# Kernel tuning notes

Hardware: AMD Instinct MI355X
Metric: run time of the kernel (lower is better)

## Reference

```python
import jax, jax.numpy as jnp
import numpy as np

K = 3          # kernel_size
DEG_P = 6      # numerator coeffs (order 5)
DEG_Q = 4      # denominator coeffs (powers 1..4)


def setup_inputs() -> dict:
    key = jax.random.key(0)
    k1, k2, k3 = jax.random.split(key, 3)
    B, Cin, Cout, H, W = 4, 16, 16, 64, 64
    x = jax.random.normal(k1, (B, Cin, H, W), dtype=jnp.float32)
    # per (out_channel f, in_channel c, kernel position p) rational coefficients
    A = jax.random.normal(k2, (Cout, Cin, K * K, DEG_P), dtype=jnp.float32) * 0.1
    Bc = jax.random.normal(k3, (Cout, Cin, K * K, DEG_Q), dtype=jnp.float32) * 0.1
    return {"x": x, "A": A, "Bc": Bc}


def reference(x, A, Bc):
    # x: [B, C, H, W]; A: [F, C, K*K, 6]; Bc: [F, C, K*K, 4]
    B, C, H, W = x.shape
    pad = (K - 1) // 2
    xp = jnp.pad(x, ((0, 0), (0, 0), (pad, pad), (pad, pad)))
    # sliding windows, one slice per kernel offset -> [K*K, B, C, H, W]
    wins = jnp.stack([xp[:, :, i:i + H, j:j + W]
                      for i in range(K) for j in range(K)])
    # powers x^0..x^5 -> [K*K, B, C, H, W, 6]
    pw = wins[..., None] ** jnp.arange(DEG_P, dtype=x.dtype)
    P = jnp.einsum('pbchwi,fcpi->fpbchw', pw, A)
    Q = 1.0 + jnp.abs(jnp.einsum('pbchwi,fcpi->fpbchw', pw[..., 1:1 + DEG_Q], Bc))
    # sum over kernel positions (p) and input channels (c) -> [F, B, H, W]
    out = jnp.sum(P / Q, axis=(1, 3))
    return jnp.transpose(out, (1, 0, 2, 3))  # [B, F, H, W]
```

## Files before the change

### kernel.cpp

```cpp
#include <hip/hip_runtime.h>


#define BB   4
#define CIN  16
#define COUT 16
#define HH   64
#define WW   64

__global__ __launch_bounds__(1024, 8) void KAConv_kernel(
    const float* __restrict__ x,
    const float* __restrict__ A,
    const float* __restrict__ Bc,
    float* __restrict__ out)
{
    const int blk = blockIdx.x;
    const int f   = blk & 15;
    const int rp  = (blk >> 4) & 31;
    const int b   = blk >> 9;

    const int tid  = threadIdx.x;
    const int cw   = __builtin_amdgcn_readfirstlane(tid >> 6);
    const int lane = tid & 63;
    const int w    = lane;
    const int r0   = rp << 1;

    const float* __restrict__ Ac = A  + (f * CIN + cw) * 54;
    const float* __restrict__ Bq = Bc + (f * CIN + cw) * 36;
    const float* __restrict__ xc = x  + (b * CIN + cw) * (HH * WW);

    float vv[4][3];
    #pragma unroll
    for (int ri = 0; ri < 4; ++ri) {
        const int hh   = r0 - 1 + ri;
        const bool okh = (hh >= 0) & (hh < HH);
        #pragma unroll
        for (int j = 0; j < 3; ++j) {
            const int wj  = w + j - 1;
            const bool ok = okh & (wj >= 0) & (wj < WW);
            vv[ri][j] = ok ? xc[hh * WW + wj] : 0.0f;
        }
    }

    float acc0 = 0.0f, acc1 = 0.0f;

    #pragma unroll
    for (int p = 0; p < 9; ++p) {
        const int i = p / 3;
        const int j = p % 3;
        const float va = vv[i][j];
        const float vb = vv[i + 1][j];
        const float a0 = Ac[p * 6 + 0], a1 = Ac[p * 6 + 1], a2 = Ac[p * 6 + 2];
        const float a3 = Ac[p * 6 + 3], a4 = Ac[p * 6 + 4], a5 = Ac[p * 6 + 5];
        const float b1 = Bq[p * 4 + 0], b2 = Bq[p * 4 + 1];
        const float b3 = Bq[p * 4 + 2], b4 = Bq[p * 4 + 3];

        float P0 = a5, P1 = a5;
        P0 = fmaf(P0, va, a4);  P1 = fmaf(P1, vb, a4);
        P0 = fmaf(P0, va, a3);  P1 = fmaf(P1, vb, a3);
        P0 = fmaf(P0, va, a2);  P1 = fmaf(P1, vb, a2);
        P0 = fmaf(P0, va, a1);  P1 = fmaf(P1, vb, a1);
        P0 = fmaf(P0, va, a0);  P1 = fmaf(P1, vb, a0);

        float q0 = b4, q1 = b4;
        q0 = fmaf(q0, va, b3);  q1 = fmaf(q1, vb, b3);
        q0 = fmaf(q0, va, b2);  q1 = fmaf(q1, vb, b2);
        q0 = fmaf(q0, va, b1);  q1 = fmaf(q1, vb, b1);
        q0 *= va;               q1 *= vb;

        const float d0 = 1.0f + fabsf(q0);
        const float d1 = 1.0f + fabsf(q1);
        acc0 = fmaf(P0, __builtin_amdgcn_rcpf(d0), acc0);
        acc1 = fmaf(P1, __builtin_amdgcn_rcpf(d1), acc1);
    }

    __shared__ float sRed[CIN][128];
    sRed[cw][lane]      = acc0;
    sRed[cw][64 + lane] = acc1;
    __syncthreads();

    if (tid < 128) {
        float s = 0.0f;
        #pragma unroll
        for (int k = 0; k < CIN; ++k) s += sRed[k][tid];
        const int row = r0 + (tid >> 6);
        const int col = tid & 63;
        out[((b * COUT + f) * HH + row) * WW + col] = s;
    }
}

extern "C" void kernel_launch(void* const* d_in, const int* in_sizes, int n_in,
                              void* d_out, int out_size, void* d_ws, size_t ws_size,
                              hipStream_t stream) {
    const float* x  = (const float*)d_in[0];
    const float* A  = (const float*)d_in[1];
    const float* Bc = (const float*)d_in[2];
    float* out = (float*)d_out;

    const int grid = BB * (HH / 2) * COUT;
    KAConv_kernel<<<grid, 1024, 0, stream>>>(x, A, Bc, out);
}
```

Measured before the change: 19.97 us.

## Pair rational terms over common denominator and widen per-block row tiling

Each block now computes 8 output rows with 512 threads, and each wave processes two input channels over a 10-row register window, so loaded input rows are reused across rows. Pairs of kernel-position terms are combined as (PA*dB+PB*dA)/(dA*dB), which roughly halves the reciprocal instructions. This adds a few multiplies and may raise register pressure. It also risks precision loss or overflow in the product of denominators for large inputs.

Measured after the change: 23.38 us. +17.1%, slower.

```diff
diff --git a/kernel.cpp b/kernel.cpp
--- a/kernel.cpp
+++ b/kernel.cpp
@@ -7,7 +7,24 @@
 #define HH   64
 #define WW   64
 
-__global__ __launch_bounds__(1024, 8) void KAConv_kernel(
+static __device__ __forceinline__ void rat(const float* __restrict__ Ac,
+                                           const float* __restrict__ Bq,
+                                           int p, float v, float& P, float& d)
+{
+    const float a0 = Ac[p*6+0], a1 = Ac[p*6+1], a2 = Ac[p*6+2];
+    const float a3 = Ac[p*6+3], a4 = Ac[p*6+4], a5 = Ac[p*6+5];
+    const float b1 = Bq[p*4+0], b2 = Bq[p*4+1], b3 = Bq[p*4+2], b4 = Bq[p*4+3];
+    float Pp = a5;
+    Pp = fmaf(Pp, v, a4); Pp = fmaf(Pp, v, a3); Pp = fmaf(Pp, v, a2);
+    Pp = fmaf(Pp, v, a1); Pp = fmaf(Pp, v, a0);
+    float q = b4;
+    q = fmaf(q, v, b3); q = fmaf(q, v, b2); q = fmaf(q, v, b1);
+    q *= v;
+    P = Pp;
+    d = 1.0f + fabsf(q);
+}
+
+__global__ __launch_bounds__(512, 4) void KAConv_kernel(
     const float* __restrict__ x,
     const float* __restrict__ A,
     const float* __restrict__ Bc,
@@ -15,76 +32,82 @@
 {
     const int blk = blockIdx.x;
     const int f   = blk & 15;
-    const int rp  = (blk >> 4) & 31;
-    const int b   = blk >> 9;
+    const int rg  = (blk >> 4) & 7;
+    const int b   = blk >> 7;
 
-    const int tid  = threadIdx.x;
-    const int cw   = __builtin_amdgcn_readfirstlane(tid >> 6);
-    const int lane = tid & 63;
-    const int w    = lane;
-    const int r0   = rp << 1;
+    const int tid   = threadIdx.x;
+    const int wid   = __builtin_amdgcn_readfirstlane(tid >> 6);
+    const int lane  = tid & 63;
+    const int w     = lane;
+    const int rbase = rg << 3;
 
-    const float* __restrict__ Ac = A  + (f * CIN + cw) * 54;
-    const float* __restrict__ Bq = Bc + (f * CIN + cw) * 36;
-    const float* __restrict__ xc = x  + (b * CIN + cw) * (HH * WW);
+    __shared__ float sRed[8][512];
 
-    float vv[4][3];
+    float acc[8];
     #pragma unroll
-    for (int ri = 0; ri < 4; ++ri) {
-        const int hh   = r0 - 1 + ri;
-        const bool okh = (hh >= 0) & (hh < HH);
+    for (int i = 0; i < 8; ++i) acc[i] = 0.0f;
+
+    #pragma unroll 1
+    for (int half = 0; half < 2; ++half) {
+        const int c = wid + (half << 3);
+        const float* __restrict__ Ac = A  + (f * CIN + c) * 54;
+        const float* __restrict__ Bq = Bc + (f * CIN + c) * 36;
+        const float* __restrict__ xc = x  + (b * CIN + c) * (HH * WW);
+
+        float win[10][3];
         #pragma unroll
-        for (int j = 0; j < 3; ++j) {
-            const int wj  = w + j - 1;
-            const bool ok = okh & (wj >= 0) & (wj < WW);
-            vv[ri][j] = ok ? xc[hh * WW + wj] : 0.0f;
+        for (int r = 0; r < 10; ++r) {
+            const int hh   = rbase - 1 + r;
+            const bool okh = (hh >= 0) & (hh < HH);
+            #pragma unroll
+            for (int j = 0; j < 3; ++j) {
+                const int wj  = w + j - 1;
+                const bool ok = okh & (wj >= 0) & (wj < WW);
+                win[r][j] = ok ? xc[hh * WW + wj] : 0.0f;
+            }
+        }
+
+        #pragma unroll
+        for (int rp = 0; rp < 4; ++rp) {
+            #pragma unroll
+            for (int px = 0; px < 2; ++px) {
+                float aloc = 0.0f;
+                #pragma unroll
+                for (int pp = 0; pp < 4; ++pp) {
+                    const int pA = 2 * pp, pB = 2 * pp + 1;
+                    const float vA = win[(rp << 1) + px + pA / 3][pA % 3];
+                    const float vB = win[(rp << 1) + px + pB / 3][pB % 3];
+                    float PA, dA, PB, dB;
+                    rat(Ac, Bq, pA, vA, PA, dA);
+                    rat(Ac, Bq, pB, vB, PB, dB);
+                    float num = PA * dB;
+                    num = fmaf(PB, dA, num);
+                    const float den = dA * dB;
+                    aloc = fmaf(num, __builtin_amdgcn_rcpf(den), aloc);
+                }
+                {
+                    const float v8 = win[(rp << 1) + px + 2][2];
+                    float P8, d8;
+                    rat(Ac, Bq, 8, v8, P8, d8);
+                    aloc = fmaf(P8, __builtin_amdgcn_rcpf(d8), aloc);
+                }
+                acc[(rp << 1) + px] += aloc;
+            }
         }
     }
 
-    float acc0 = 0.0f, acc1 = 0.0f;
-
     #pragma unroll
-    for (int p = 0; p < 9; ++p) {
-        const int i = p / 3;
-        const int j = p % 3;
-        const float va = vv[i][j];
-        const float vb = vv[i + 1][j];
-        const float a0 = Ac[p * 6 + 0], a1 = Ac[p * 6 + 1], a2 = Ac[p * 6 + 2];
-        const float a3 = Ac[p * 6 + 3], a4 = Ac[p * 6 + 4], a5 = Ac[p * 6 + 5];
-        const float b1 = Bq[p * 4 + 0], b2 = Bq[p * 4 + 1];
-        const float b3 = Bq[p * 4 + 2], b4 = Bq[p * 4 + 3];
-
-        float P0 = a5, P1 = a5;
-        P0 = fmaf(P0, va, a4);  P1 = fmaf(P1, vb, a4);
-        P0 = fmaf(P0, va, a3);  P1 = fmaf(P1, vb, a3);
-        P0 = fmaf(P0, va, a2);  P1 = fmaf(P1, vb, a2);
-        P0 = fmaf(P0, va, a1);  P1 = fmaf(P1, vb, a1);
-        P0 = fmaf(P0, va, a0);  P1 = fmaf(P1, vb, a0);
-
-        float q0 = b4, q1 = b4;
-        q0 = fmaf(q0, va, b3);  q1 = fmaf(q1, vb, b3);
-        q0 = fmaf(q0, va, b2);  q1 = fmaf(q1, vb, b2);
-        q0 = fmaf(q0, va, b1);  q1 = fmaf(q1, vb, b1);
-        q0 *= va;               q1 *= vb;
-
-        const float d0 = 1.0f + fabsf(q0);
-        const float d1 = 1.0f + fabsf(q1);
-        acc0 = fmaf(P0, __builtin_amdgcn_rcpf(d0), acc0);
-        acc1 = fmaf(P1, __builtin_amdgcn_rcpf(d1), acc1);
-    }
-
-    __shared__ float sRed[CIN][128];
-    sRed[cw][lane]      = acc0;
-    sRed[cw][64 + lane] = acc1;
+    for (int rl = 0; rl < 8; ++rl)
+        sRed[wid][rl * 64 + lane] = acc[rl];
     __syncthreads();
 
-    if (tid < 128) {
+    {
         float s = 0.0f;
         #pragma unroll
-        for (int k = 0; k < CIN; ++k) s += sRed[k][tid];
-        const int row = r0 + (tid >> 6);
+        for (int k = 0; k < 8; ++k) s += sRed[k][tid];
+        const int rl  = tid >> 6;
         const int col = tid & 63;
-        out[((b * COUT + f) * HH + row) * WW + col] = s;
+        out[((b * COUT + f) * HH + rbase + rl) * WW + col] = s;
     }
 }
 
@@ -96,6 +119,6 @@
     const float* Bc = (const float*)d_in[2];
     float* out = (float*)d_out;
 
-    const int grid = BB * (HH / 2) * COUT;
-    KAConv_kernel<<<grid, 1024, 0, stream>>>(x, A, Bc, out);
+    const int grid = BB * (HH / 8) * COUT;
+    KAConv_kernel<<<grid, 512, 0, stream>>>(x, A, Bc, out);
 }
```

## Tile two output channels and four input channels per thread to reuse window loads

Applied to the files above, without the earlier changes.

Each block now covers 2 output channels and 8 rows. Each thread loops over 4 input channels and computes both output channels from the same loaded 3x4 input window. This halves the global x loads per output, shrinks the grid from 2048 to 256 blocks, and cuts the shared-memory reduction from 16 partials to 4 per output, with all 1024 threads writing outputs. The cost is more serial work per thread and fewer blocks (256), which may underfill the GPU's CUs, and launch bounds are relaxed to 4 blocks per CU.

Result: slower. 20.57 us (+3.0%).

```diff
diff --git a/kernel.cpp b/kernel.cpp
--- a/kernel.cpp
+++ b/kernel.cpp
@@ -7,83 +7,122 @@
 #define HH   64
 #define WW   64
 
-__global__ __launch_bounds__(1024, 8) void KAConv_kernel(
+__global__ __launch_bounds__(1024, 4) void KAConv_kernel(
     const float* __restrict__ x,
     const float* __restrict__ A,
     const float* __restrict__ Bc,
     float* __restrict__ out)
 {
     const int blk = blockIdx.x;
-    const int f   = blk & 15;
-    const int rp  = (blk >> 4) & 31;
-    const int b   = blk >> 9;
+    const int fp  = blk >> 5;
+    const int b   = (blk >> 3) & 3;
+    const int rt  = blk & 7;
 
     const int tid  = threadIdx.x;
-    const int cw   = __builtin_amdgcn_readfirstlane(tid >> 6);
-    const int lane = tid & 63;
-    const int w    = lane;
-    const int r0   = rp << 1;
+    const int team = __builtin_amdgcn_readfirstlane(tid >> 8);
+    const int tp   = tid & 255;
+    const int w    = tp & 63;
+    const int r0   = (rt << 3) + ((tp >> 6) << 1);
+    const int c0   = team << 2;
+    const int f0   = fp << 1;
 
-    const float* __restrict__ Ac = A  + (f * CIN + cw) * 54;
-    const float* __restrict__ Bq = Bc + (f * CIN + cw) * 36;
-    const float* __restrict__ xc = x  + (b * CIN + cw) * (HH * WW);
+    const float* __restrict__ xb  = x  + (b * CIN + c0) * (HH * WW);
+    const float* __restrict__ pA0 = A  + (f0 * CIN + c0) * 54;
+    const float* __restrict__ pB0 = Bc + (f0 * CIN + c0) * 36;
+    const float* __restrict__ pA1 = pA0 + CIN * 54;
+    const float* __restrict__ pB1 = pB0 + CIN * 36;
 
-    float vv[4][3];
-    #pragma unroll
-    for (int ri = 0; ri < 4; ++ri) {
-        const int hh   = r0 - 1 + ri;
-        const bool okh = (hh >= 0) & (hh < HH);
+    float acc00 = 0.0f, acc01 = 0.0f;
+    float acc10 = 0.0f, acc11 = 0.0f;
+
+    #pragma unroll 1
+    for (int c = 0; c < 4; ++c) {
+        const float* __restrict__ xc = xb + c * (HH * WW);
+
+        float vv[4][3];
         #pragma unroll
-        for (int j = 0; j < 3; ++j) {
-            const int wj  = w + j - 1;
-            const bool ok = okh & (wj >= 0) & (wj < WW);
-            vv[ri][j] = ok ? xc[hh * WW + wj] : 0.0f;
+        for (int ri = 0; ri < 4; ++ri) {
+            const int hh   = r0 - 1 + ri;
+            const bool okh = (hh >= 0) & (hh < HH);
+            #pragma unroll
+            for (int j = 0; j < 3; ++j) {
+                const int wj  = w + j - 1;
+                const bool ok = okh & (wj >= 0) & (wj < WW);
+                vv[ri][j] = ok ? xc[hh * WW + wj] : 0.0f;
+            }
+        }
+
+        const float* __restrict__ Ac0 = pA0 + c * 54;
+        const float* __restrict__ Bq0 = pB0 + c * 36;
+        const float* __restrict__ Ac1 = pA1 + c * 54;
+        const float* __restrict__ Bq1 = pB1 + c * 36;
+
+        #pragma unroll
+        for (int p = 0; p < 9; ++p) {
+            const int i = p / 3, j = p % 3;
+            const float va = vv[i][j];
+            const float vb = vv[i + 1][j];
+
+            {
+                const float a0 = Ac0[p*6+0], a1 = Ac0[p*6+1], a2 = Ac0[p*6+2];
+                const float a3 = Ac0[p*6+3], a4 = Ac0[p*6+4], a5 = Ac0[p*6+5];
+                const float b1 = Bq0[p*4+0], b2 = Bq0[p*4+1];
+                const float b3 = Bq0[p*4+2], b4 = Bq0[p*4+3];
+                float P0 = a5, P1 = a5;
+                P0 = fmaf(P0, va, a4);  P1 = fmaf(P1, vb, a4);
+                P0 = fmaf(P0, va, a3);  P1 = fmaf(P1, vb, a3);
+                P0 = fmaf(P0, va, a2);  P1 = fmaf(P1, vb, a2);
+                P0 = fmaf(P0, va, a1);  P1 = fmaf(P1, vb, a1);
+                P0 = fmaf(P0, va, a0);  P1 = fmaf(P1, vb, a0);
+                float q0 = b4, q1 = b4;
+                q0 = fmaf(q0, va, b3);  q1 = fmaf(q1, vb, b3);
+                q0 = fmaf(q0, va, b2);  q1 = fmaf(q1, vb, b2);
+                q0 = fmaf(q0, va, b1);  q1 = fmaf(q1, vb, b1);
+                q0 *= va;               q1 *= vb;
+                const float d0 = 1.0f + fabsf(q0);
+                const float d1 = 1.0f + fabsf(q1);
+                acc00 = fmaf(P0, __builtin_amdgcn_rcpf(d0), acc00);
+                acc01 = fmaf(P1, __builtin_amdgcn_rcpf(d1), acc01);
+            }
+            {
+                const float a0 = Ac1[p*6+0], a1 = Ac1[p*6+1], a2 = Ac1[p*6+2];
+                const float a3 = Ac1[p*6+3], a4 = Ac1[p*6+4], a5 = Ac1[p*6+5];
+                const float b1 = Bq1[p*4+0], b2 = Bq1[p*4+1];
+                const float b3 = Bq1[p*4+2], b4 = Bq1[p*4+3];
+                float P0 = a5, P1 = a5;
+                P0 = fmaf(P0, va, a4);  P1 = fmaf(P1, vb, a4);
+                P0 = fmaf(P0, va, a3);  P1 = fmaf(P1, vb, a3);
+                P0 = fmaf(P0, va, a2);  P1 = fmaf(P1, vb, a2);
+                P0 = fmaf(P0, va, a1);  P1 = fmaf(P1, vb, a1);
+                P0 = fmaf(P0, va, a0);  P1 = fmaf(P1, vb, a0);
+                float q0 = b4, q1 = b4;
+                q0 = fmaf(q0, va, b3);  q1 = fmaf(q1, vb, b3);
+                q0 = fmaf(q0, va, b2);  q1 = fmaf(q1, vb, b2);
+                q0 = fmaf(q0, va, b1);  q1 = fmaf(q1, vb, b1);
+                q0 *= va;               q1 *= vb;
+                const float d0 = 1.0f + fabsf(q0);
+                const float d1 = 1.0f + fabsf(q1);
+                acc10 = fmaf(P0, __builtin_amdgcn_rcpf(d0), acc10);
+                acc11 = fmaf(P1, __builtin_amdgcn_rcpf(d1), acc11);
+            }
         }
     }
 
-    float acc0 = 0.0f, acc1 = 0.0f;
-
-    #pragma unroll
-    for (int p = 0; p < 9; ++p) {
-        const int i = p / 3;
-        const int j = p % 3;
-        const float va = vv[i][j];
-        const float vb = vv[i + 1][j];
-        const float a0 = Ac[p * 6 + 0], a1 = Ac[p * 6 + 1], a2 = Ac[p * 6 + 2];
-        const float a3 = Ac[p * 6 + 3], a4 = Ac[p * 6 + 4], a5 = Ac[p * 6 + 5];
-        const float b1 = Bq[p * 4 + 0], b2 = Bq[p * 4 + 1];
-        const float b3 = Bq[p * 4 + 2], b4 = Bq[p * 4 + 3];
-
-        float P0 = a5, P1 = a5;
-        P0 = fmaf(P0, va, a4);  P1 = fmaf(P1, vb, a4);
-        P0 = fmaf(P0, va, a3);  P1 = fmaf(P1, vb, a3);
-        P0 = fmaf(P0, va, a2);  P1 = fmaf(P1, vb, a2);
-        P0 = fmaf(P0, va, a1);  P1 = fmaf(P1, vb, a1);
-        P0 = fmaf(P0, va, a0);  P1 = fmaf(P1, vb, a0);
-
-        float q0 = b4, q1 = b4;
-        q0 = fmaf(q0, va, b3);  q1 = fmaf(q1, vb, b3);
-        q0 = fmaf(q0, va, b2);  q1 = fmaf(q1, vb, b2);
-        q0 = fmaf(q0, va, b1);  q1 = fmaf(q1, vb, b1);
-        q0 *= va;               q1 *= vb;
-
-        const float d0 = 1.0f + fabsf(q0);
-        const float d1 = 1.0f + fabsf(q1);
-        acc0 = fmaf(P0, __builtin_amdgcn_rcpf(d0), acc0);
-        acc1 = fmaf(P1, __builtin_amdgcn_rcpf(d1), acc1);
-    }
-
-    __shared__ float sRed[CIN][128];
-    sRed[cw][lane]      = acc0;
-    sRed[cw][64 + lane] = acc1;
+    __shared__ float sRed[4][4][256];
+    sRed[team][0][tp] = acc00;
+    sRed[team][1][tp] = acc01;
+    sRed[team][2][tp] = acc10;
+    sRed[team][3][tp] = acc11;
     __syncthreads();
 
-    if (tid < 128) {
-        float s = 0.0f;
-        #pragma unroll
-        for (int k = 0; k < CIN; ++k) s += sRed[k][tid];
-        const int row = r0 + (tid >> 6);
-        const int col = tid & 63;
+    {
+        const int q  = tid >> 8;
+        const int t2 = tid & 255;
+        const float s = sRed[0][q][t2] + sRed[1][q][t2]
+                      + sRed[2][q][t2] + sRed[3][q][t2];
+        const int row = (rt << 3) + ((t2 >> 6) << 1) + (q & 1);
+        const int f   = f0 + (q >> 1);
+        const int col = t2 & 63;
         out[((b * COUT + f) * HH + row) * WW + col] = s;
     }
 }
@@ -96,6 +135,6 @@
     const float* Bc = (const float*)d_in[2];
     float* out = (float*)d_out;
 
-    const int grid = BB * (HH / 2) * COUT;
+    const int grid = 8 * BB * 8;
     KAConv_kernel<<<grid, 1024, 0, stream>>>(x, A, Bc, out);
 }
```
